# Performance work log

Measured on AMD Instinct MI355X. Metric: run time of the kernel, lower is better.

## Reference

```python
import jax, jax.numpy as jnp
import numpy as np


def setup_inputs() -> dict:
    key = jax.random.key(0)
    k1, k2 = jax.random.split(key)
    B, H, W, D, K = 4, 256, 256, 32, 8
    inputs = jax.random.uniform(k1, (B, H, W, D), dtype=jnp.float32)
    beta = jax.random.normal(k2, (D, K), dtype=jnp.float32)
    return {"inputs": inputs, "beta": beta}


def reference(inputs, beta):
    # u[i,k] = beta[i,k]^2 / sum_k beta[i,k]^2  -- per-feature class mass distribution
    beta_sq = jnp.square(beta)
    u = beta_sq / jnp.sum(beta_sq, axis=1, keepdims=True)  # (D, K)
    # mass_prototype[b,h,w,i,k] = u[i,k] * inputs[b,h,w,i]  (outer-product broadcast)
    return inputs[..., None] * u  # (B, H, W, D, K)
```

## Files before the change

kernel.cpp:

```cpp
#include <hip/hip_runtime.h>


#define DIMD 32
#define DIMK 8

typedef float f32x4 __attribute__((ext_vector_type(4)));

__global__ __launch_bounds__(256) void mass_proto_kernel(
    const float* __restrict__ inputs,
    const float* __restrict__ beta,
    float* __restrict__ out,
    int n4)
{
    __shared__ float bsq[DIMD * DIMK];
    __shared__ float u[DIMD * DIMK];

    const int t = threadIdx.x;
    float b = beta[t];
    bsq[t] = b * b;
    __syncthreads();
    const int row = t >> 3;
    float s = 0.f;
#pragma unroll
    for (int j = 0; j < DIMK; ++j) s += bsq[row * DIMK + j];
    u[t] = bsq[t] / s;
    __syncthreads();

    const f32x4* __restrict__ u4 = reinterpret_cast<const f32x4*>(u);
    f32x4* __restrict__ out4 = reinterpret_cast<f32x4*>(out);

    const f32x4 uu = u4[t & 63];

    int idx = blockIdx.x * blockDim.x + threadIdx.x;
    const int stride = gridDim.x * blockDim.x;

    for (; idx + 3 * stride < n4; idx += 4 * stride) {
        const float x0 = inputs[(idx + 0 * stride) >> 1];
        const float x1 = inputs[(idx + 1 * stride) >> 1];
        const float x2 = inputs[(idx + 2 * stride) >> 1];
        const float x3 = inputs[(idx + 3 * stride) >> 1];

        __builtin_nontemporal_store(x0 * uu, &out4[idx + 0 * stride]);
        __builtin_nontemporal_store(x1 * uu, &out4[idx + 1 * stride]);
        __builtin_nontemporal_store(x2 * uu, &out4[idx + 2 * stride]);
        __builtin_nontemporal_store(x3 * uu, &out4[idx + 3 * stride]);
    }
    for (; idx < n4; idx += stride) {
        __builtin_nontemporal_store(inputs[idx >> 1] * uu, &out4[idx]);
    }
}

extern "C" void kernel_launch(void* const* d_in, const int* in_sizes, int n_in,
                              void* d_out, int out_size, void* d_ws, size_t ws_size,
                              hipStream_t stream) {
    const float* inputs = (const float*)d_in[0];
    const float* beta   = (const float*)d_in[1];
    float* out = (float*)d_out;

    const int n4 = out_size / 4;
    const int threads = 256;
    const int blocks = 2048;

    mass_proto_kernel<<<blocks, threads, 0, stream>>>(inputs, beta, out, n4);
}
```

Before: 60.78 us.

## Prefetch inputs as vectorized loads into LDS before computing u, fixed trip grid

Each block now loads all of its input scalars up front with 16-byte vector loads, issued before the beta/u reduction so their latency overlaps that setup. The values are staged in shared memory and read back per output chunk. The grid is resized so each thread does exactly TRIPS output stores instead of a grid-stride loop. This replaces many redundant scalar global loads (two threads per scalar) with one coalesced vector pass, at the cost of 16KB of LDS per block, which may reduce occupancy.

```diff
diff --git a/kernel.cpp b/kernel.cpp
--- a/kernel.cpp
+++ b/kernel.cpp
@@ -3,6 +3,7 @@
 
 #define DIMD 32
 #define DIMK 8
+#define TRIPS 32
 
 typedef float f32x4 __attribute__((ext_vector_type(4)));
 
@@ -10,12 +11,35 @@
     const float* __restrict__ inputs,
     const float* __restrict__ beta,
     float* __restrict__ out,
-    int n4)
+    int n4,
+    int nelem4)
 {
+    __shared__ __align__(16) float u[DIMD * DIMK];
     __shared__ float bsq[DIMD * DIMK];
-    __shared__ float u[DIMD * DIMK];
+    __shared__ __align__(16) float xin[TRIPS * 128];
 
     const int t = threadIdx.x;
+    const int stride  = gridDim.x * blockDim.x;
+    const int estride4 = stride >> 3;
+
+    const f32x4* __restrict__ in4 = reinterpret_cast<const f32x4*>(inputs);
+    f32x4 v0, v1, v2, v3;
+    {
+        const int base = blockIdx.x * 32 + (t & 31);
+        const int j0 = (0 * 256 + t) >> 5;
+        const int j1 = (1 * 256 + t) >> 5;
+        const int j2 = (2 * 256 + t) >> 5;
+        const int j3 = (3 * 256 + t) >> 5;
+        int g0 = base + j0 * estride4;
+        int g1 = base + j1 * estride4;
+        int g2 = base + j2 * estride4;
+        int g3 = base + j3 * estride4;
+        v0 = (g0 < nelem4) ? in4[g0] : (f32x4)0.f;
+        v1 = (g1 < nelem4) ? in4[g1] : (f32x4)0.f;
+        v2 = (g2 < nelem4) ? in4[g2] : (f32x4)0.f;
+        v3 = (g3 < nelem4) ? in4[g3] : (f32x4)0.f;
+    }
+
     float b = beta[t];
     bsq[t] = b * b;
     __syncthreads();
@@ -24,29 +48,27 @@
 #pragma unroll
     for (int j = 0; j < DIMK; ++j) s += bsq[row * DIMK + j];
     u[t] = bsq[t] / s;
+
+    f32x4* xin4 = reinterpret_cast<f32x4*>(xin);
+    xin4[0 * 256 + t] = v0;
+    xin4[1 * 256 + t] = v1;
+    xin4[2 * 256 + t] = v2;
+    xin4[3 * 256 + t] = v3;
     __syncthreads();
 
     const f32x4* __restrict__ u4 = reinterpret_cast<const f32x4*>(u);
+    const f32x4 uu = u4[t & 63];
     f32x4* __restrict__ out4 = reinterpret_cast<f32x4*>(out);
 
-    const f32x4 uu = u4[t & 63];
-
-    int idx = blockIdx.x * blockDim.x + threadIdx.x;
-    const int stride = gridDim.x * blockDim.x;
-
-    for (; idx + 3 * stride < n4; idx += 4 * stride) {
-        const float x0 = inputs[(idx + 0 * stride) >> 1];
-        const float x1 = inputs[(idx + 1 * stride) >> 1];
-        const float x2 = inputs[(idx + 2 * stride) >> 1];
-        const float x3 = inputs[(idx + 3 * stride) >> 1];
-
-        __builtin_nontemporal_store(x0 * uu, &out4[idx + 0 * stride]);
-        __builtin_nontemporal_store(x1 * uu, &out4[idx + 1 * stride]);
-        __builtin_nontemporal_store(x2 * uu, &out4[idx + 2 * stride]);
-        __builtin_nontemporal_store(x3 * uu, &out4[idx + 3 * stride]);
-    }
-    for (; idx < n4; idx += stride) {
-        __builtin_nontemporal_store(inputs[idx >> 1] * uu, &out4[idx]);
+    const int idx = blockIdx.x * blockDim.x + t;
+    const int th = t >> 1;
+#pragma unroll 4
+    for (int j = 0; j < TRIPS; ++j) {
+        const int c = idx + j * stride;
+        if (c < n4) {
+            const float x = xin[j * 128 + th];
+            __builtin_nontemporal_store(x * uu, &out4[c]);
+        }
     }
 }
 
@@ -59,7 +81,8 @@
 
     const int n4 = out_size / 4;
     const int threads = 256;
-    const int blocks = 2048;
+    const int blocks = (n4 + threads * TRIPS - 1) / (threads * TRIPS);
+    const int nelem4 = (out_size / DIMK) / 4;
 
-    mass_proto_kernel<<<blocks, threads, 0, stream>>>(inputs, beta, out, n4);
+    mass_proto_kernel<<<blocks, threads, 0, stream>>>(inputs, beta, out, n4, nelem4);
 }
```

After: 68.08 us. 12.0% more time.
